# Kernel optimization log

Measured on AMD Instinct MI355X. Metric: run time of the kernel, lower is better.

Reference implementation:

```python
import jax, jax.numpy as jnp
import numpy as np

N = 100000
E = 1600000
IN_F = 128
OUT_F = 32
HEADS = 6
NEG_SLOPE = 0.2


def setup_inputs() -> dict:
    key = jax.random.key(0)
    k1, k2, k3, k4, k5 = jax.random.split(key, 5)
    x = jax.random.normal(k1, (N, IN_F), dtype=jnp.float32)
    edge_index = jax.random.randint(k2, (2, E), 0, N, dtype=jnp.int64)
    # GATConv params (PyG layout): shared linear for src/dst, per-head attention vectors, bias
    glorot = lambda k, shape: jax.random.normal(k, shape, dtype=jnp.float32) * np.sqrt(2.0 / (shape[0] + shape[-1]))
    W = glorot(k3, (IN_F, HEADS * OUT_F))          # lin.weight^T
    att_src = glorot(k4, (HEADS, OUT_F)) * 0.1     # [H, C]
    att_dst = glorot(k5, (HEADS, OUT_F)) * 0.1
    bias = jnp.zeros((OUT_F,), dtype=jnp.float32)  # concat=False -> bias of size out_feature
    return {"x": x, "edge_index": edge_index, "W": W,
            "att_src": att_src, "att_dst": att_dst, "bias": bias}


def reference(x, edge_index, W, att_src, att_dst, bias):
    src, dst = edge_index[0], edge_index[1]
    # Linear projection to per-head features: [N, H, C]
    xp = (x @ W).reshape(N, HEADS, OUT_F)
    # Per-node attention logit halves: [N, H]
    a_s = jnp.einsum("nhc,hc->nh", xp, att_src)
    a_d = jnp.einsum("nhc,hc->nh", xp, att_dst)
    # Per-edge logits with LeakyReLU: [E, H]
    e = jax.nn.leaky_relu(a_s[src] + a_d[dst], negative_slope=NEG_SLOPE)
    # Segment softmax over edges grouped by destination node
    m = jax.ops.segment_max(e, dst, num_segments=N)            # [N, H]
    m = jnp.where(jnp.isfinite(m), m, 0.0)                     # empty segments -> -inf guard
    e = jnp.exp(e - m[dst])
    s = jax.ops.segment_sum(e, dst, num_segments=N)            # [N, H]
    alpha = e / (s[dst] + 1e-16)                               # [E, H]
    # Weighted scatter-add aggregation: [N, H, C]
    msg = xp[src] * alpha[:, :, None]
    out = jax.ops.segment_sum(msg, dst, num_segments=N)
    # concat=False -> mean over heads, add bias, then SELU
    out = out.mean(axis=1) + bias
    return jax.nn.selu(out)
```

## Files before the change

kernel.cpp:

```cpp
#include <hip/hip_runtime.h>


typedef __attribute__((ext_vector_type(8))) short short8;
typedef __attribute__((ext_vector_type(4))) float f32x4;

#define SK 136
#define SLOTS 48

__device__ __forceinline__ unsigned short f2bf(float f)
{
    unsigned int u = __float_as_uint(f);
    u = (u + 0x7fffu + ((u >> 16) & 1u)) >> 16;
    return (unsigned short)u;
}

__global__ __launch_bounds__(256) void k_prep(
    const float* __restrict__ W,
    const float* __restrict__ att_src, const float* __restrict__ att_dst,
    unsigned short* __restrict__ wat, unsigned short* __restrict__ Wb,
    int* __restrict__ deg, int N)
{
    int i = blockIdx.x * 256 + threadIdx.x;
    if (i < N) deg[i] = 0;
    if (i < 128 * 192) Wb[i] = f2bf(W[i]);
    if (i < 128 * 16) {
        int k = i >> 4, c = i & 15;
        float v = 0.f;
        if (c < 12) {
            int h = c < 6 ? c : c - 6;
            const float* av = (c < 6 ? att_src : att_dst) + h * 32;
            const float* wr = W + k * 192 + h * 32;
            #pragma unroll
            for (int j = 0; j < 32; ++j) v = fmaf(wr[j], av[j], v);
        }
        wat[i] = f2bf(v);
    }
}

__global__ __launch_bounds__(256) void k_gd(
    const float* __restrict__ x, const unsigned short* __restrict__ Wb,
    const unsigned short* __restrict__ wat,
    unsigned short* __restrict__ xpb, float* __restrict__ a_s, float* __restrict__ a_d,
    const int* __restrict__ ei, int* __restrict__ deg, int* __restrict__ csr,
    int N, int E, int GB, int DB)
{
    __shared__ __align__(16) unsigned short xt[64 * SK];
    const int t   = threadIdx.x;
    const int bid = (int)blockIdx.x >> 1;

    if (blockIdx.x & 1) {
        if (bid >= DB) return;
        const int G = DB * 256;
        const int gid = bid * 256 + t;
        int s[4], d[4], r[4];
        #pragma unroll
        for (int k = 0; k < 4; ++k) {
            int e = gid + k * G;
            bool ok = e < E;
            int ec = ok ? e : 0;
            s[k] = ei[ec];
            d[k] = ei[E + ec];
            if (!ok) d[k] = -1;
        }
        #pragma unroll
        for (int k = 0; k < 4; ++k)
            r[k] = (d[k] >= 0) ? atomicAdd(&deg[d[k]], 1) : SLOTS;
        #pragma unroll
        for (int k = 0; k < 4; ++k)
            if (r[k] < SLOTS && d[k] >= 0) csr[d[k] * SLOTS + r[k]] = s[k];
        return;
    }

    if (bid >= GB) return;
    const int wave = t >> 6;
    const int lane = t & 63;
    const int ln   = lane & 15;
    const int q    = lane >> 4;
    const int n0   = bid * 64;
    const int cb   = wave * 48;

    {
        const float4* x4 = (const float4*)x;
        #pragma unroll
        for (int it = 0; it < 8; ++it) {
            int i   = t + it * 256;
            int row = i >> 5;
            int c4  = i & 31;
            int gr  = n0 + row;
            if (gr > N - 1) gr = N - 1;
            float4 f = x4[(size_t)gr * 32 + c4];
            unsigned int u0 = (unsigned int)f2bf(f.x) | ((unsigned int)f2bf(f.y) << 16);
            unsigned int u1 = (unsigned int)f2bf(f.z) | ((unsigned int)f2bf(f.w) << 16);
            *(uint2*)(xt + row * SK + c4 * 4) = make_uint2(u0, u1);
        }
    }

    short8 bw[3][4];
    #pragma unroll
    for (int nt = 0; nt < 3; ++nt)
        #pragma unroll
        for (int kbi = 0; kbi < 4; ++kbi) {
            short8 v;
            #pragma unroll
            for (int j = 0; j < 8; ++j)
                v[j] = (short)Wb[(kbi * 32 + q * 8 + j) * 192 + cb + nt * 16 + ln];
            bw[nt][kbi] = v;
        }
    short8 bwa[4];
    #pragma unroll
    for (int kbi = 0; kbi < 4; ++kbi) {
        short8 v;
        #pragma unroll
        for (int j = 0; j < 8; ++j)
            v[j] = (short)wat[(kbi * 32 + q * 8 + j) * 16 + ln];
        bwa[kbi] = v;
    }

    __syncthreads();

    f32x4 acc[4][3];
    #pragma unroll
    for (int mt = 0; mt < 4; ++mt)
        #pragma unroll
        for (int nt = 0; nt < 3; ++nt) acc[mt][nt] = (f32x4)0.f;

    #pragma unroll
    for (int kbi = 0; kbi < 4; ++kbi) {
        #pragma unroll
        for (int mt = 0; mt < 4; ++mt) {
            short8 av = *(const short8*)(xt + (mt * 16 + ln) * SK + kbi * 32 + q * 8);
            #pragma unroll
            for (int nt = 0; nt < 3; ++nt)
                acc[mt][nt] = __builtin_amdgcn_mfma_f32_16x16x32_bf16(
                    av, bw[nt][kbi], acc[mt][nt], 0, 0, 0);
        }
    }

    f32x4 acca = (f32x4)0.f;
    #pragma unroll
    for (int kbi = 0; kbi < 4; ++kbi) {
        short8 av = *(const short8*)(xt + (wave * 16 + ln) * SK + kbi * 32 + q * 8);
        acca = __builtin_amdgcn_mfma_f32_16x16x32_bf16(av, bwa[kbi], acca, 0, 0, 0);
    }

    #pragma unroll
    for (int mt = 0; mt < 4; ++mt) {
        #pragma unroll
        for (int r = 0; r < 4; ++r) {
            int grow = n0 + mt * 16 + q * 4 + r;
            if (grow < N) {
                #pragma unroll
                for (int nt = 0; nt < 3; ++nt)
                    xpb[(size_t)grow * 192 + cb + nt * 16 + ln] = f2bf(acc[mt][nt][r]);
            }
        }
    }
    #pragma unroll
    for (int r = 0; r < 4; ++r) {
        int grow = n0 + wave * 16 + q * 4 + r;
        if (grow < N) {
            if (ln < 6)       a_s[(size_t)grow * 6 + ln]     = acca[r];
            else if (ln < 12) a_d[(size_t)grow * 6 + ln - 6] = acca[r];
        }
    }
}

__global__ __launch_bounds__(256) void k_agg(
    const unsigned short* __restrict__ xpb,
    const float* __restrict__ a_s, const float* __restrict__ a_d,
    const int* __restrict__ csr, const int* __restrict__ degv,
    const float* __restrict__ bias, float* __restrict__ out, int N)
{
    const int wid = threadIdx.x >> 6;
    const int l   = threadIdx.x & 63;
    const int n = blockIdx.x * 4 + wid;
    if (n >= N) return;

    int deg = degv[n];
    deg = deg < SLOTS ? deg : SLOTS;
    const int nb  = n * SLOTS;
    const int hr  = l >> 3;
    const int h   = hr < 6 ? hr : 5;
    const int lc  = l < 48 ? l : 47;
    const unsigned lcb = (unsigned)lc * 8u;
    const unsigned h4  = (unsigned)h * 4u;
    const char* __restrict__ xpB = (const char*)xpb;
    const char* __restrict__ asB = (const char*)a_s;

    const float zd = a_d[(size_t)n * 6 + h];

    float ax = 0.f, ay = 0.f, az = 0.f, aw = 0.f, se = 0.f;

    int my3 = (l < deg) ? csr[nb + l] * 3 : 0;
    int i = 0;
    for (; i + 8 <= deg; i += 8) {
        unsigned s3[8]; float as[8]; uint2 xv[8];
        #pragma unroll
        for (int k = 0; k < 8; ++k) {
            s3[k] = (unsigned)__shfl(my3, i + k);
            as[k] = *(const float*)(asB + s3[k] * 8u + h4);
        }
        #pragma unroll
        for (int k = 0; k < 8; ++k)
            xv[k] = *(const uint2*)(xpB + s3[k] * 128u + lcb);
        #pragma unroll
        for (int k = 0; k < 8; ++k) {
            float z = as[k] + zd;
            z = z > 0.f ? z : 0.2f * z;
            float ev = __expf(z);
            ax = fmaf(ev, __uint_as_float(xv[k].x << 16), ax);
            ay = fmaf(ev, __uint_as_float(xv[k].x & 0xffff0000u), ay);
            az = fmaf(ev, __uint_as_float(xv[k].y << 16), az);
            aw = fmaf(ev, __uint_as_float(xv[k].y & 0xffff0000u), aw);
            se += ev;
        }
    }
    for (; i < deg; ++i) {
        unsigned s3 = (unsigned)__shfl(my3, i);
        float z  = *(const float*)(asB + s3 * 8u + h4) + zd;
        z = z > 0.f ? z : 0.2f * z;
        float ev = __expf(z);
        uint2 xv = *(const uint2*)(xpB + s3 * 128u + lcb);
        ax = fmaf(ev, __uint_as_float(xv.x << 16), ax);
        ay = fmaf(ev, __uint_as_float(xv.x & 0xffff0000u), ay);
        az = fmaf(ev, __uint_as_float(xv.y << 16), az);
        aw = fmaf(ev, __uint_as_float(xv.y & 0xffff0000u), aw);
        se += ev;
    }

    const float inv = 1.f / (se + 1e-16f);
    float v0 = (l < 48) ? ax * inv : 0.f;
    float v1 = (l < 48) ? ay * inv : 0.f;
    float v2 = (l < 48) ? az * inv : 0.f;
    float v3 = (l < 48) ? aw * inv : 0.f;

    #pragma unroll
    for (int d = 8; d <= 32; d <<= 1) {
        v0 += __shfl_down(v0, d);
        v1 += __shfl_down(v1, d);
        v2 += __shfl_down(v2, d);
        v3 += __shfl_down(v3, d);
    }

    if (l < 8) {
        float4 b4 = ((const float4*)bias)[l];
        const float sc = 1.0507009873554805f, al = 1.6732632423543772f;
        float m[4] = {v0 * (1.f / 6.f) + b4.x, v1 * (1.f / 6.f) + b4.y,
                      v2 * (1.f / 6.f) + b4.z, v3 * (1.f / 6.f) + b4.w};
        #pragma unroll
        for (int k = 0; k < 4; ++k)
            m[k] = m[k] > 0.f ? sc * m[k] : sc * al * (__expf(m[k]) - 1.f);
        ((float4*)out)[(size_t)n * 8 + l] = make_float4(m[0], m[1], m[2], m[3]);
    }
}

extern "C" void kernel_launch(void* const* d_in, const int* in_sizes, int n_in,
                              void* d_out, int out_size, void* d_ws, size_t ws_size,
                              hipStream_t stream)
{
    const float* x       = (const float*)d_in[0];
    const int*   ei      = (const int*)d_in[1];
    const float* W       = (const float*)d_in[2];
    const float* att_src = (const float*)d_in[3];
    const float* att_dst = (const float*)d_in[4];
    const float* bias    = (const float*)d_in[5];
    float* out = (float*)d_out;

    const int N = in_sizes[0] / 128;
    const int E = in_sizes[1] / 2;
    const int GB = (N + 63) / 64;
    const int DB = (E + 4 * 256 - 1) / (4 * 256);
    const int MB = (GB > DB ? GB : DB) * 2;

    char* ws = (char*)d_ws;
    size_t o = 0;
    auto take = [&](size_t bytes) { size_t r = o; o = (o + bytes + 255) & ~(size_t)255; return r; };
    unsigned short* xpb = (unsigned short*)(ws + take((size_t)N * 192 * 2));
    float* a_s     = (float*)(ws + take((size_t)N * 6 * 4));
    float* a_d     = (float*)(ws + take((size_t)N * 6 * 4));
    int*   deg     = (int*)  (ws + take((size_t)N * 4));
    int*   csr     = (int*)  (ws + take((size_t)N * SLOTS * 4));
    unsigned short* wat = (unsigned short*)(ws + take((size_t)128 * 16 * 2));
    unsigned short* Wb  = (unsigned short*)(ws + take((size_t)128 * 192 * 2));
    (void)ws_size; (void)n_in; (void)out_size;

    int pg = (N + 255) / 256;
    k_prep<<<pg, 256, 0, stream>>>(W, att_src, att_dst, wat, Wb, deg, N);
    k_gd<<<MB, 256, 0, stream>>>(x, Wb, wat, xpb, a_s, a_d,
                                 ei, deg, csr, N, E, GB, DB);
    k_agg<<<(N + 3) / 4, 256, 0, stream>>>(xpb, a_s, a_d, csr, deg, bias, out, N);
}
```

Measured before the change: 281.3 us.

## Quantize projected features to int8 with per-node per-head scales

The projected node features are stored as int8 with a per-row, per-head absmax scale instead of bf16. The projection kernel computes the scales through shared-memory atomics, and the aggregation kernel dequantizes by folding the scale into the attention weight. This halves the bytes gathered per edge in the memory-bound aggregation. In exchange it adds an extra scale load per edge, extra syncs and reductions in the projection kernel, and lower precision in the features.

```diff
diff --git a/kernel.cpp b/kernel.cpp
--- a/kernel.cpp
+++ b/kernel.cpp
@@ -40,11 +40,13 @@
 __global__ __launch_bounds__(256) void k_gd(
     const float* __restrict__ x, const unsigned short* __restrict__ Wb,
     const unsigned short* __restrict__ wat,
-    unsigned short* __restrict__ xpb, float* __restrict__ a_s, float* __restrict__ a_d,
+    char* __restrict__ xpb, float* __restrict__ sc,
+    float* __restrict__ a_s, float* __restrict__ a_d,
     const int* __restrict__ ei, int* __restrict__ deg, int* __restrict__ csr,
     int N, int E, int GB, int DB)
 {
     __shared__ __align__(16) unsigned short xt[64 * SK];
+    __shared__ unsigned int smax[64 * 6];
     const int t   = threadIdx.x;
     const int bid = (int)blockIdx.x >> 1;
 
@@ -93,6 +95,7 @@
             unsigned int u1 = (unsigned int)f2bf(f.z) | ((unsigned int)f2bf(f.w) << 16);
             *(uint2*)(xt + row * SK + c4 * 4) = make_uint2(u0, u1);
         }
+        if (t < 128) { smax[t] = 0u; smax[t + 128] = 0u; smax[t + 256] = 0u; }
     }
 
     short8 bw[3][4];
@@ -147,11 +150,17 @@
     for (int mt = 0; mt < 4; ++mt) {
         #pragma unroll
         for (int r = 0; r < 4; ++r) {
-            int grow = n0 + mt * 16 + q * 4 + r;
-            if (grow < N) {
+            int row = mt * 16 + q * 4 + r;
+            #pragma unroll
+            for (int nt = 0; nt < 3; ++nt) {
+                float m = fabsf(acc[mt][nt][r]);
                 #pragma unroll
-                for (int nt = 0; nt < 3; ++nt)
-                    xpb[(size_t)grow * 192 + cb + nt * 16 + ln] = f2bf(acc[mt][nt][r]);
+                for (int d = 1; d <= 8; d <<= 1)
+                    m = fmaxf(m, __shfl_xor(m, d));
+                if (ln == 0) {
+                    int head = (cb + nt * 16) >> 5;
+                    atomicMax(&smax[row * 6 + head], __float_as_uint(m));
+                }
             }
         }
     }
@@ -163,10 +172,38 @@
             else if (ln < 12) a_d[(size_t)grow * 6 + ln - 6] = acca[r];
         }
     }
+    __syncthreads();
+
+    for (int i2 = t; i2 < 384; i2 += 256) {
+        int row = i2 / 6, h = i2 - row * 6;
+        float m = __uint_as_float(smax[i2]);
+        int grow = n0 + row;
+        if (grow < N) sc[(size_t)grow * 6 + h] = m * (1.f / 127.f);
+        smax[i2] = __float_as_uint(m > 0.f ? 127.f / m : 0.f);
+    }
+    __syncthreads();
+
+    #pragma unroll
+    for (int mt = 0; mt < 4; ++mt) {
+        #pragma unroll
+        for (int r = 0; r < 4; ++r) {
+            int row  = mt * 16 + q * 4 + r;
+            int grow = n0 + row;
+            if (grow < N) {
+                #pragma unroll
+                for (int nt = 0; nt < 3; ++nt) {
+                    int head = (cb + nt * 16) >> 5;
+                    float inv = __uint_as_float(smax[row * 6 + head]);
+                    int qv = (int)rintf(acc[mt][nt][r] * inv);
+                    xpb[(size_t)grow * 192 + cb + nt * 16 + ln] = (char)qv;
+                }
+            }
+        }
+    }
 }
 
 __global__ __launch_bounds__(256) void k_agg(
-    const unsigned short* __restrict__ xpb,
+    const char* __restrict__ xpb, const float* __restrict__ sc,
     const float* __restrict__ a_s, const float* __restrict__ a_d,
     const int* __restrict__ csr, const int* __restrict__ degv,
     const float* __restrict__ bias, float* __restrict__ out, int N)
@@ -182,10 +219,11 @@
     const int hr  = l >> 3;
     const int h   = hr < 6 ? hr : 5;
     const int lc  = l < 48 ? l : 47;
-    const unsigned lcb = (unsigned)lc * 8u;
+    const unsigned lcb = (unsigned)lc * 4u;
     const unsigned h4  = (unsigned)h * 4u;
     const char* __restrict__ xpB = (const char*)xpb;
     const char* __restrict__ asB = (const char*)a_s;
+    const char* __restrict__ scB = (const char*)sc;
 
     const float zd = a_d[(size_t)n * 6 + h];
 
@@ -194,37 +232,49 @@
     int my3 = (l < deg) ? csr[nb + l] * 3 : 0;
     int i = 0;
     for (; i + 8 <= deg; i += 8) {
-        unsigned s3[8]; float as[8]; uint2 xv[8];
+        unsigned s3[8]; float as[8]; float ss[8]; unsigned int xv[8];
         #pragma unroll
         for (int k = 0; k < 8; ++k) {
             s3[k] = (unsigned)__shfl(my3, i + k);
             as[k] = *(const float*)(asB + s3[k] * 8u + h4);
+            ss[k] = *(const float*)(scB + s3[k] * 8u + h4);
         }
         #pragma unroll
         for (int k = 0; k < 8; ++k)
-            xv[k] = *(const uint2*)(xpB + s3[k] * 128u + lcb);
+            xv[k] = *(const unsigned int*)(xpB + s3[k] * 64u + lcb);
         #pragma unroll
         for (int k = 0; k < 8; ++k) {
             float z = as[k] + zd;
-            z = z > 0.f ? z : 0.2f * z;
+            z = fmaxf(z, 0.2f * z);
             float ev = __expf(z);
-            ax = fmaf(ev, __uint_as_float(xv[k].x << 16), ax);
-            ay = fmaf(ev, __uint_as_float(xv[k].x & 0xffff0000u), ay);
-            az = fmaf(ev, __uint_as_float(xv[k].y << 16), az);
-            aw = fmaf(ev, __uint_as_float(xv[k].y & 0xffff0000u), aw);
+            float evs = ev * ss[k];
+            unsigned v = xv[k];
+            float f0 = (float)((int)(v << 24) >> 24);
+            float f1 = (float)((int)(v << 16) >> 24);
+            float f2 = (float)((int)(v <<  8) >> 24);
+            float f3 = (float)((int)v >> 24);
+            ax = fmaf(evs, f0, ax);
+            ay = fmaf(evs, f1, ay);
+            az = fmaf(evs, f2, az);
+            aw = fmaf(evs, f3, aw);
             se += ev;
         }
     }
     for (; i < deg; ++i) {
         unsigned s3 = (unsigned)__shfl(my3, i);
         float z  = *(const float*)(asB + s3 * 8u + h4) + zd;
-        z = z > 0.f ? z : 0.2f * z;
+        z = fmaxf(z, 0.2f * z);
         float ev = __expf(z);
-        uint2 xv = *(const uint2*)(xpB + s3 * 128u + lcb);
-        ax = fmaf(ev, __uint_as_float(xv.x << 16), ax);
-        ay = fmaf(ev, __uint_as_float(xv.x & 0xffff0000u), ay);
-        az = fmaf(ev, __uint_as_float(xv.y << 16), az);
-        aw = fmaf(ev, __uint_as_float(xv.y & 0xffff0000u), aw);
+        float evs = ev * *(const float*)(scB + s3 * 8u + h4);
+        unsigned v = *(const unsigned int*)(xpB + s3 * 64u + lcb);
+        float f0 = (float)((int)(v << 24) >> 24);
+        float f1 = (float)((int)(v << 16) >> 24);
+        float f2 = (float)((int)(v <<  8) >> 24);
+        float f3 = (float)((int)v >> 24);
+        ax = fmaf(evs, f0, ax);
+        ay = fmaf(evs, f1, ay);
+        az = fmaf(evs, f2, az);
+        aw = fmaf(evs, f3, aw);
         se += ev;
     }
 
@@ -244,12 +294,12 @@
 
     if (l < 8) {
         float4 b4 = ((const float4*)bias)[l];
-        const float sc = 1.0507009873554805f, al = 1.6732632423543772f;
+        const float scs = 1.0507009873554805f, al = 1.6732632423543772f;
         float m[4] = {v0 * (1.f / 6.f) + b4.x, v1 * (1.f / 6.f) + b4.y,
                       v2 * (1.f / 6.f) + b4.z, v3 * (1.f / 6.f) + b4.w};
         #pragma unroll
         for (int k = 0; k < 4; ++k)
-            m[k] = m[k] > 0.f ? sc * m[k] : sc * al * (__expf(m[k]) - 1.f);
+            m[k] = m[k] > 0.f ? scs * m[k] : scs * al * (__expf(m[k]) - 1.f);
         ((float4*)out)[(size_t)n * 8 + l] = make_float4(m[0], m[1], m[2], m[3]);
     }
 }
@@ -275,7 +325,8 @@
     char* ws = (char*)d_ws;
     size_t o = 0;
     auto take = [&](size_t bytes) { size_t r = o; o = (o + bytes + 255) & ~(size_t)255; return r; };
-    unsigned short* xpb = (unsigned short*)(ws + take((size_t)N * 192 * 2));
+    char*  xpb     = (char*) (ws + take((size_t)N * 192));
+    float* sc      = (float*)(ws + take((size_t)N * 6 * 4));
     float* a_s     = (float*)(ws + take((size_t)N * 6 * 4));
     float* a_d     = (float*)(ws + take((size_t)N * 6 * 4));
     int*   deg     = (int*)  (ws + take((size_t)N * 4));
@@ -286,7 +337,7 @@
 
     int pg = (N + 255) / 256;
     k_prep<<<pg, 256, 0, stream>>>(W, att_src, att_dst, wat, Wb, deg, N);
-    k_gd<<<MB, 256, 0, stream>>>(x, Wb, wat, xpb, a_s, a_d,
+    k_gd<<<MB, 256, 0, stream>>>(x, Wb, wat, xpb, sc, a_s, a_d,
                                  ei, deg, csr, N, E, GB, DB);
-    k_agg<<<(N + 3) / 4, 256, 0, stream>>>(xpb, a_s, a_d, csr, deg, bias, out, N);
-}
+    k_agg<<<(N + 3) / 4, 256, 0, stream>>>(xpb, sc, a_s, a_d, csr, deg, bias, out, N);
+}
```

Result: no change. 277.2 us (-1.5%).
